# Performance work log

Measured on AMD Instinct MI355X. Metric: run time of the kernel, lower is better.

## Reference

```python
import jax, jax.numpy as jnp
import numpy as np

B, S, HID = 1, 2048, 4096
NH, NKV = 32, 8
HD = HID // NH          # 128
N_REP = NH // NKV       # 4
ROPE_THETA = 10000.0


def setup_inputs() -> dict:
    key = jax.random.key(0)
    ks = jax.random.split(key, 5)
    scale = 0.02
    x = jax.random.normal(ks[0], (B, S, HID), dtype=jnp.float32)
    Wq = jax.random.normal(ks[1], (HID, HID), dtype=jnp.float32) * scale
    Wk = jax.random.normal(ks[2], (NKV * HD, HID), dtype=jnp.float32) * scale
    Wv = jax.random.normal(ks[3], (NKV * HD, HID), dtype=jnp.float32) * scale
    Wo = jax.random.normal(ks[4], (HID, HID), dtype=jnp.float32) * scale
    position_ids = jnp.broadcast_to(jnp.arange(S, dtype=jnp.int32)[None, :], (B, S))
    return {"x": x, "Wq": Wq, "Wk": Wk, "Wv": Wv, "Wo": Wo, "position_ids": position_ids}


def _rope_cache(seq_len, dtype):
    inv_freq = 1.0 / (ROPE_THETA ** (jnp.arange(0, HD, 2, dtype=jnp.float32) / HD))
    t = jnp.arange(seq_len, dtype=jnp.float32)
    freqs = t[:, None] * inv_freq[None, :]            # [S, HD/2]
    emb = jnp.concatenate([freqs, freqs], axis=-1)    # [S, HD]
    return jnp.cos(emb).astype(dtype), jnp.sin(emb).astype(dtype)


def _rotate_half(x):
    x1, x2 = x[..., : HD // 2], x[..., HD // 2:]
    return jnp.concatenate([-x2, x1], axis=-1)


def reference(x, Wq, Wk, Wv, Wo, position_ids):
    b, s, _ = x.shape
    # projections (nn.Linear: x @ W.T)
    q = (x @ Wq.T).reshape(b, s, NH, HD).transpose(0, 2, 1, 3)    # [B,NH,S,HD]
    k = (x @ Wk.T).reshape(b, s, NKV, HD).transpose(0, 2, 1, 3)   # [B,NKV,S,HD]
    v = (x @ Wv.T).reshape(b, s, NKV, HD).transpose(0, 2, 1, 3)
    # RoPE
    cos_c, sin_c = _rope_cache(s, x.dtype)
    cos = cos_c[position_ids][:, None, :, :]   # [B,1,S,HD]
    sin = sin_c[position_ids][:, None, :, :]
    q = q * cos + _rotate_half(q) * sin
    k = k * cos + _rotate_half(k) * sin
    # GQA repeat_kv
    k = jnp.repeat(k, N_REP, axis=1)   # [B,NH,S,HD]
    v = jnp.repeat(v, N_REP, axis=1)
    # scaled dot-product attention with causal mask
    scores = jnp.einsum('bhqd,bhkd->bhqk', q, k) / jnp.sqrt(jnp.float32(HD))
    causal = jnp.tril(jnp.ones((s, s), dtype=bool))
    scores = jnp.where(causal[None, None, :, :], scores, jnp.finfo(scores.dtype).min)
    attn = jax.nn.softmax(scores.astype(jnp.float32), axis=-1).astype(q.dtype)
    out = jnp.einsum('bhqk,bhkd->bhqd', attn, v)                  # [B,NH,S,HD]
    out = out.transpose(0, 2, 1, 3).reshape(b, s, NH * HD)
    return out @ Wo.T
```

## Files before the change

kernel.cpp:

```cpp
#include <hip/hip_runtime.h>
#include <hip/hip_bf16.h>

#define DEVI __device__ __forceinline__

typedef __attribute__((ext_vector_type(8))) __bf16 bf16x8;
typedef __attribute__((ext_vector_type(4))) float f32x4;

DEVI f32x4 mfma_16x16x32(bf16x8 a, bf16x8 b, f32x4 c) {
  return __builtin_amdgcn_mfma_f32_16x16x32_bf16(a, b, c, 0, 0, 0);
}

DEVI void gld16(const void* g, void* l) {
  __builtin_amdgcn_global_load_lds(
      reinterpret_cast<const __attribute__((address_space(1))) unsigned int*>(
          reinterpret_cast<unsigned long long>(g)),
      reinterpret_cast<__attribute__((address_space(3))) unsigned int*>(
          reinterpret_cast<unsigned long long>(l)),
      16, 0, 0);
}

DEVI unsigned short f2bf(float f) {
  unsigned u = __builtin_bit_cast(unsigned, f);
  u += 0x7FFFu + ((u >> 16) & 1u);
  return (unsigned short)(u >> 16);
}
DEVI float bf2f(unsigned short b) {
  return __builtin_bit_cast(float, (unsigned)b << 16);
}

struct Conv5 {
  const float4 *x, *wq, *wk, *wv, *wo;
  ushort4 *xb, *wqkv, *wob;
};
__global__ void k_conv_all(Conv5 a) {
  constexpr int C0 = 2097152;
  constexpr int C1 = C0 + 4194304;
  constexpr int C2 = C1 + 1048576;
  constexpr int C3 = C2 + 1048576;
  constexpr int C4 = C3 + 4194304;
  int stride = gridDim.x * blockDim.x;
  for (int i = blockIdx.x * blockDim.x + threadIdx.x; i < C4; i += stride) {
    const float4* src; ushort4* dst; int j;
    if (i < C0)      { src = a.x;  dst = a.xb;             j = i; }
    else if (i < C1) { src = a.wq; dst = a.wqkv;           j = i - C0; }
    else if (i < C2) { src = a.wk; dst = a.wqkv + 4194304; j = i - C1; }
    else if (i < C3) { src = a.wv; dst = a.wqkv + 5242880; j = i - C2; }
    else             { src = a.wo; dst = a.wob;            j = i - C3; }
    float4 v = src[j];
    ushort4 o; o.x = f2bf(v.x); o.y = f2bf(v.y); o.z = f2bf(v.z); o.w = f2bf(v.w);
    dst[j] = o;
  }
}

__global__ void k_rope_table(float2* __restrict__ tab) {
  int idx = blockIdx.x * blockDim.x + threadIdx.x;
  int s = idx >> 6, d = idx & 63;
  float invf = powf(10000.0f, -(float)d * (1.0f / 64.0f));
  float f = (float)s * invf;
  tab[idx] = make_float2(cosf(f), sinf(f));
}

template <int NH_, int L2NH>
__global__ void k_rope_v(unsigned short* __restrict__ X, const float2* __restrict__ tab,
                         const int* __restrict__ pos, float scale) {
  int t = blockIdx.x * blockDim.x + threadIdx.x;
  int d0 = (t & 7) * 8;
  int sh = t >> 3;
  int s  = sh >> L2NH;
  int h  = sh & (NH_ - 1);
  size_t base = (size_t)s * (NH_ * 128) + h * 128 + d0;
  const float4* tf = (const float4*)(tab + (size_t)pos[s] * 64 + d0);
  unsigned short a[8], b[8], oa[8], ob[8];
  *(ushort4*)&a[0] = *(const ushort4*)(X + base);
  *(ushort4*)&a[4] = *(const ushort4*)(X + base + 4);
  *(ushort4*)&b[0] = *(const ushort4*)(X + base + 64);
  *(ushort4*)&b[4] = *(const ushort4*)(X + base + 68);
#pragma unroll
  for (int j = 0; j < 4; ++j) {
    float4 cs = tf[j];
    float x1 = bf2f(a[2*j]),   x2 = bf2f(b[2*j]);
    float y1 = bf2f(a[2*j+1]), y2 = bf2f(b[2*j+1]);
    oa[2*j]   = f2bf((x1 * cs.x - x2 * cs.y) * scale);
    ob[2*j]   = f2bf((x2 * cs.x + x1 * cs.y) * scale);
    oa[2*j+1] = f2bf((y1 * cs.z - y2 * cs.w) * scale);
    ob[2*j+1] = f2bf((y2 * cs.z + y1 * cs.w) * scale);
  }
  *(ushort4*)(X + base)      = *(ushort4*)&oa[0];
  *(ushort4*)(X + base + 4)  = *(ushort4*)&oa[4];
  *(ushort4*)(X + base + 64) = *(ushort4*)&ob[0];
  *(ushort4*)(X + base + 68) = *(ushort4*)&ob[4];
}

template <int EPI>
__global__ __launch_bounds__(256, 2)
void k_gemm64(const unsigned short* __restrict__ A,
              const unsigned short* __restrict__ B,
              void* __restrict__ Cp,
              unsigned short* __restrict__ Kp,
              unsigned short* __restrict__ Vtp,
              int K) {
  __shared__ __align__(16) unsigned short As[128][64];
  __shared__ __align__(16) unsigned short Bs[128][64];
  const int tid  = threadIdx.x;
  const int lane = tid & 63;
  const int wave = tid >> 6;
  const int bm = blockIdx.y * 128;
  const int bn = blockIdx.x * 128;
  const int wm = (wave >> 1) * 64;
  const int wn = (wave & 1) * 64;
  const int l15 = lane & 15;
  const int lg  = lane >> 4;

  f32x4 acc[4][4] = {};

  const int srow  = lane >> 3;
  const int scol  = ((lane & 7) ^ srow) * 8;
  const unsigned short* aS = A + (size_t)(bm + wave * 32 + srow) * K + scol;
  const unsigned short* bS = B + (size_t)(bn + wave * 32 + srow) * K + scol;

  for (int k0 = 0; k0 < K; k0 += 64) {
    __syncthreads();
#pragma unroll
    for (int c = 0; c < 4; ++c) {
      gld16(aS + (size_t)(c * 8) * K + k0, &As[wave * 32 + c * 8][0]);
      gld16(bS + (size_t)(c * 8) * K + k0, &Bs[wave * 32 + c * 8][0]);
    }
    __syncthreads();

#pragma unroll
    for (int ks = 0; ks < 2; ++ks) {
      bf16x8 a[4], b[4];
#pragma unroll
      for (int m = 0; m < 4; ++m)
        a[m] = *(const bf16x8*)&As[wm + m * 16 + l15][((ks * 4 + lg) ^ (l15 & 7)) * 8];
#pragma unroll
      for (int n = 0; n < 4; ++n)
        b[n] = *(const bf16x8*)&Bs[wn + n * 16 + l15][((ks * 4 + lg) ^ (l15 & 7)) * 8];
#pragma unroll
      for (int m = 0; m < 4; ++m)
#pragma unroll
        for (int n = 0; n < 4; ++n)
          acc[m][n] = mfma_16x16x32(a[m], b[n], acc[m][n]);
    }
  }

#pragma unroll
  for (int m = 0; m < 4; ++m)
#pragma unroll
    for (int n = 0; n < 4; ++n)
#pragma unroll
      for (int r = 0; r < 4; ++r) {
        int row = bm + wm + m * 16 + lg * 4 + r;
        int col = bn + wn + n * 16 + l15;
        float v = acc[m][n][r];
        if (EPI == 0) {
          if (col < 4096)      ((unsigned short*)Cp)[(size_t)row * 4096 + col] = f2bf(v);
          else if (col < 5120) Kp[(size_t)row * 1024 + (col - 4096)] = f2bf(v);
          else                 Vtp[(size_t)(col - 5120) * 2048 + row] = f2bf(v);
        } else {
          ((float*)Cp)[(size_t)row * 4096 + col] = v;
        }
      }
}

__global__ __launch_bounds__(256, 2)
void k_attn(const unsigned short* __restrict__ Q,
            const unsigned short* __restrict__ Kb,
            const unsigned short* __restrict__ Vt,
            unsigned short* __restrict__ AO) {
  __shared__ __align__(16) unsigned short Kl[2][64][128];
  __shared__ __align__(16) unsigned short Vl[2][128][64];
  __shared__ __align__(16) unsigned short Pl[4][16][72];
  const int tid = threadIdx.x, lane = tid & 63, w = tid >> 6;
  const int bid = blockIdx.x;
  const int qi = 31 - (bid >> 5);
  const int h  = bid & 31;
  const int q0 = qi * 64;
  const int kh = h >> 2;
  const int l15 = lane & 15, lg = lane >> 4;

  bf16x8 qf[4];
  {
    const unsigned short* qr = Q + (size_t)(q0 + w * 16 + l15) * 4096 + h * 128;
#pragma unroll
    for (int ks = 0; ks < 4; ++ks) qf[ks] = *(const bf16x8*)(qr + ks * 32 + lg * 8);
  }

  f32x4 o[8] = {};
  float m_run = -1e30f, l_run = 0.f;
  const int nkb = qi + 1;
  const int myq = q0 + w * 16 + l15;

  auto stageK = [&](int buf, int kv0) {
#pragma unroll
    for (int c = 0; c < 4; ++c) {
      int row = 16 * w + 4 * c + lg;
      gld16(Kb + (size_t)(kv0 + row) * 1024 + kh * 128 + ((l15 ^ (row & 7)) * 8),
            &Kl[buf][16 * w + 4 * c][0]);
    }
  };
  auto stageV = [&](int buf, int kv0) {
#pragma unroll
    for (int c = 0; c < 4; ++c) {
      int row = 32 * w + 8 * c + (lane >> 3);
      gld16(Vt + (size_t)(kh * 128 + row) * 2048 + kv0 + (((lane & 7) ^ (row & 7)) * 8),
            &Vl[buf][32 * w + 8 * c][0]);
    }
  };

  stageK(0, 0);
  stageV(0, 0);
  int cur = 0;

  for (int kb = 0; kb < nkb; ++kb) {
    const int kv0 = kb * 64;
    __syncthreads();
    if (kb + 1 < nkb) { stageK(cur ^ 1, kv0 + 64); stageV(cur ^ 1, kv0 + 64); }

    f32x4 s[4] = {};
    __builtin_amdgcn_s_setprio(1);
#pragma unroll
    for (int ks = 0; ks < 4; ++ks)
#pragma unroll
      for (int n = 0; n < 4; ++n) {
        bf16x8 bk = *(const bf16x8*)&Kl[cur][n * 16 + l15][((ks * 4 + lg) ^ (l15 & 7)) * 8];
        s[n] = mfma_16x16x32(bk, qf[ks], s[n]);
      }
    __builtin_amdgcn_s_setprio(0);

    if (kb == nkb - 1) {
#pragma unroll
      for (int n = 0; n < 4; ++n)
#pragma unroll
        for (int r = 0; r < 4; ++r)
          if (kv0 + n * 16 + lg * 4 + r > myq) s[n][r] = -1e30f;
    }

    float mx = -1e30f;
#pragma unroll
    for (int n = 0; n < 4; ++n)
      mx = fmaxf(mx, fmaxf(fmaxf(s[n][0], s[n][1]), fmaxf(s[n][2], s[n][3])));
    mx = fmaxf(mx, __shfl_xor(mx, 16));
    mx = fmaxf(mx, __shfl_xor(mx, 32));

    if (!__all(mx <= m_run + 8.0f)) {
      float mn = fmaxf(m_run, mx);
      float fac = __expf(m_run - mn);
      m_run = mn;
      l_run *= fac;
#pragma unroll
      for (int j = 0; j < 8; ++j) {
        o[j][0] *= fac; o[j][1] *= fac; o[j][2] *= fac; o[j][3] *= fac;
      }
    }
    float rs = 0.f;
#pragma unroll
    for (int n = 0; n < 4; ++n)
#pragma unroll
      for (int r = 0; r < 4; ++r) {
        float pv = __expf(s[n][r] - m_run);
        s[n][r] = pv;
        rs += pv;
      }
    rs += __shfl_xor(rs, 16);
    rs += __shfl_xor(rs, 32);
    l_run += rs;

#pragma unroll
    for (int n = 0; n < 4; ++n) {
      ushort4 pk;
      pk.x = f2bf(s[n][0]); pk.y = f2bf(s[n][1]); pk.z = f2bf(s[n][2]); pk.w = f2bf(s[n][3]);
      *(ushort4*)&Pl[w][l15][n * 16 + lg * 4] = pk;
    }
    asm volatile("s_waitcnt lgkmcnt(0)" ::: "memory");
    bf16x8 pa0 = *(const bf16x8*)&Pl[w][l15][lg * 8];
    bf16x8 pa1 = *(const bf16x8*)&Pl[w][l15][32 + lg * 8];

    __builtin_amdgcn_s_setprio(1);
#pragma unroll
    for (int j = 0; j < 8; ++j) {
      bf16x8 bv0 = *(const bf16x8*)&Vl[cur][j * 16 + l15][(lg ^ (l15 & 7)) * 8];
      bf16x8 bv1 = *(const bf16x8*)&Vl[cur][j * 16 + l15][((4 + lg) ^ (l15 & 7)) * 8];
      o[j] = mfma_16x16x32(bv0, pa0, o[j]);
      o[j] = mfma_16x16x32(bv1, pa1, o[j]);
    }
    __builtin_amdgcn_s_setprio(0);
    cur ^= 1;
  }

  float inv = 1.0f / l_run;
  __syncthreads();
  unsigned short* Ol = &Kl[0][0][0];
#pragma unroll
  for (int j = 0; j < 8; ++j)
#pragma unroll
    for (int r = 0; r < 4; ++r)
      Ol[w * 2176 + l15 * 136 + j * 16 + lg * 4 + r] = f2bf(o[j][r] * inv);
  asm volatile("s_waitcnt lgkmcnt(0)" ::: "memory");
#pragma unroll
  for (int p = 0; p < 4; ++p) {
    int row = p * 4 + lg;
    bf16x8 vv = *(const bf16x8*)&Ol[w * 2176 + row * 136 + l15 * 8];
    *(bf16x8*)(AO + (size_t)(q0 + w * 16 + row) * 4096 + h * 128 + l15 * 8) = vv;
  }
}

extern "C" void kernel_launch(void* const* d_in, const int* in_sizes, int n_in,
                              void* d_out, int out_size, void* d_ws, size_t ws_size,
                              hipStream_t stream) {
  const float* x  = (const float*)d_in[0];
  const float* Wq = (const float*)d_in[1];
  const float* Wk = (const float*)d_in[2];
  const float* Wv = (const float*)d_in[3];
  const float* Wo = (const float*)d_in[4];
  const int*   pos = (const int*)d_in[5];
  float* out = (float*)d_out;

  char* p = (char*)d_ws;
  unsigned short* xb   = (unsigned short*)p; p += (size_t)2048 * 4096 * 2;
  unsigned short* wqkv = (unsigned short*)p; p += (size_t)6144 * 4096 * 2;
  unsigned short* wob  = (unsigned short*)p; p += (size_t)4096 * 4096 * 2;
  unsigned short* qb   = (unsigned short*)p; p += (size_t)2048 * 4096 * 2;
  unsigned short* kb   = (unsigned short*)p; p += (size_t)2048 * 1024 * 2;
  unsigned short* vtb  = (unsigned short*)p; p += (size_t)1024 * 2048 * 2;
  unsigned short* aob  = (unsigned short*)p; p += (size_t)2048 * 4096 * 2;
  float2*         tab  = (float2*)p;         p += (size_t)2048 * 64 * 8;

  Conv5 ca;
  ca.x  = (const float4*)x;  ca.wq = (const float4*)Wq; ca.wk = (const float4*)Wk;
  ca.wv = (const float4*)Wv; ca.wo = (const float4*)Wo;
  ca.xb = (ushort4*)xb; ca.wqkv = (ushort4*)wqkv; ca.wob = (ushort4*)wob;
  k_conv_all<<<4096, 256, 0, stream>>>(ca);
  k_rope_table<<<512, 256, 0, stream>>>(tab);

  k_gemm64<0><<<dim3(48, 16), 256, 0, stream>>>(xb, wqkv, qb, kb, vtb, 4096);

  const float scale = 0.08838834764831845f;
  k_rope_v<32, 5><<<2048, 256, 0, stream>>>(qb, tab, pos, scale);
  k_rope_v<8, 3><<<512, 256, 0, stream>>>(kb, tab, pos, 1.0f);

  k_attn<<<1024, 256, 0, stream>>>(qb, kb, vtb, aob);

  k_gemm64<1><<<dim3(32, 16), 256, 0, stream>>>(aob, wob, out, nullptr, nullptr, 4096);
}
```

Before: 479.7 us.

## Process two 64-row query tiles per attention block to reuse staged K/V tiles

Each attention workgroup now handles 128 query rows as two 64-row halves that share every K/V tile staged in LDS. This halves the LDS staging and global K/V traffic per query row and halves the grid size. The first half skips its MFMAs on the final, fully masked key block. The P scratch buffer also gets an XOR swizzle in place of padding. The cost is doubled accumulator registers, which may hurt occupancy under launch_bounds(256,2), and fewer blocks (512) with more uneven causal work per block.

```diff
diff --git a/kernel.cpp b/kernel.cpp
--- a/kernel.cpp
+++ b/kernel.cpp
@@ -170,26 +170,32 @@
             unsigned short* __restrict__ AO) {
   __shared__ __align__(16) unsigned short Kl[2][64][128];
   __shared__ __align__(16) unsigned short Vl[2][128][64];
-  __shared__ __align__(16) unsigned short Pl[4][16][72];
+  __shared__ __align__(16) unsigned short Pl[4][2][16][64];
   const int tid = threadIdx.x, lane = tid & 63, w = tid >> 6;
   const int bid = blockIdx.x;
-  const int qi = 31 - (bid >> 5);
+  const int qi = 15 - (bid >> 5);
   const int h  = bid & 31;
-  const int q0 = qi * 64;
+  const int q0 = qi * 128;
   const int kh = h >> 2;
   const int l15 = lane & 15, lg = lane >> 4;
-
-  bf16x8 qf[4];
+  const int swz = (l15 & 7);
+
+  bf16x8 qf0[4], qf1[4];
   {
-    const unsigned short* qr = Q + (size_t)(q0 + w * 16 + l15) * 4096 + h * 128;
-#pragma unroll
-    for (int ks = 0; ks < 4; ++ks) qf[ks] = *(const bf16x8*)(qr + ks * 32 + lg * 8);
-  }
-
-  f32x4 o[8] = {};
-  float m_run = -1e30f, l_run = 0.f;
-  const int nkb = qi + 1;
-  const int myq = q0 + w * 16 + l15;
+    const unsigned short* qr0 = Q + (size_t)(q0 + w * 16 + l15) * 4096 + h * 128;
+    const unsigned short* qr1 = qr0 + (size_t)64 * 4096;
+#pragma unroll
+    for (int ks = 0; ks < 4; ++ks) {
+      qf0[ks] = *(const bf16x8*)(qr0 + ks * 32 + lg * 8);
+      qf1[ks] = *(const bf16x8*)(qr1 + ks * 32 + lg * 8);
+    }
+  }
+
+  f32x4 o0[8] = {}, o1[8] = {};
+  float m0 = -1e30f, l0 = 0.f, m1 = -1e30f, l1 = 0.f;
+  const int nkb  = 2 * qi + 2;
+  const int myq0 = q0 + w * 16 + l15;
+  const int myq1 = myq0 + 64;
 
   auto stageK = [&](int buf, int kv0) {
 #pragma unroll
@@ -217,91 +223,150 @@
     __syncthreads();
     if (kb + 1 < nkb) { stageK(cur ^ 1, kv0 + 64); stageV(cur ^ 1, kv0 + 64); }
 
-    f32x4 s[4] = {};
+    const bool skip0 = (kb == nkb - 1);
+    const bool maskt = (kb >= nkb - 2);
+
+    f32x4 s0[4] = {}, s1[4] = {};
     __builtin_amdgcn_s_setprio(1);
 #pragma unroll
     for (int ks = 0; ks < 4; ++ks)
 #pragma unroll
       for (int n = 0; n < 4; ++n) {
-        bf16x8 bk = *(const bf16x8*)&Kl[cur][n * 16 + l15][((ks * 4 + lg) ^ (l15 & 7)) * 8];
-        s[n] = mfma_16x16x32(bk, qf[ks], s[n]);
+        bf16x8 bk = *(const bf16x8*)&Kl[cur][n * 16 + l15][((ks * 4 + lg) ^ swz) * 8];
+        if (!skip0) s0[n] = mfma_16x16x32(bk, qf0[ks], s0[n]);
+        s1[n] = mfma_16x16x32(bk, qf1[ks], s1[n]);
       }
     __builtin_amdgcn_s_setprio(0);
 
-    if (kb == nkb - 1) {
-#pragma unroll
-      for (int n = 0; n < 4; ++n)
-#pragma unroll
-        for (int r = 0; r < 4; ++r)
-          if (kv0 + n * 16 + lg * 4 + r > myq) s[n][r] = -1e30f;
-    }
-
-    float mx = -1e30f;
-#pragma unroll
-    for (int n = 0; n < 4; ++n)
-      mx = fmaxf(mx, fmaxf(fmaxf(s[n][0], s[n][1]), fmaxf(s[n][2], s[n][3])));
-    mx = fmaxf(mx, __shfl_xor(mx, 16));
-    mx = fmaxf(mx, __shfl_xor(mx, 32));
-
-    if (!__all(mx <= m_run + 8.0f)) {
-      float mn = fmaxf(m_run, mx);
-      float fac = __expf(m_run - mn);
-      m_run = mn;
-      l_run *= fac;
-#pragma unroll
-      for (int j = 0; j < 8; ++j) {
-        o[j][0] *= fac; o[j][1] *= fac; o[j][2] *= fac; o[j][3] *= fac;
-      }
-    }
-    float rs = 0.f;
-#pragma unroll
-    for (int n = 0; n < 4; ++n)
-#pragma unroll
-      for (int r = 0; r < 4; ++r) {
-        float pv = __expf(s[n][r] - m_run);
-        s[n][r] = pv;
-        rs += pv;
-      }
-    rs += __shfl_xor(rs, 16);
-    rs += __shfl_xor(rs, 32);
-    l_run += rs;
-
-#pragma unroll
-    for (int n = 0; n < 4; ++n) {
-      ushort4 pk;
-      pk.x = f2bf(s[n][0]); pk.y = f2bf(s[n][1]); pk.z = f2bf(s[n][2]); pk.w = f2bf(s[n][3]);
-      *(ushort4*)&Pl[w][l15][n * 16 + lg * 4] = pk;
+    if (maskt) {
+#pragma unroll
+      for (int n = 0; n < 4; ++n)
+#pragma unroll
+        for (int r = 0; r < 4; ++r) {
+          int kv = kv0 + n * 16 + lg * 4 + r;
+          if (!skip0 && kv > myq0) s0[n][r] = -1e30f;
+          if (kv > myq1)           s1[n][r] = -1e30f;
+        }
+    }
+
+    if (!skip0) {
+      float mx = -1e30f;
+#pragma unroll
+      for (int n = 0; n < 4; ++n)
+        mx = fmaxf(mx, fmaxf(fmaxf(s0[n][0], s0[n][1]), fmaxf(s0[n][2], s0[n][3])));
+      mx = fmaxf(mx, __shfl_xor(mx, 16));
+      mx = fmaxf(mx, __shfl_xor(mx, 32));
+      if (!__all(mx <= m0 + 8.0f)) {
+        float mn = fmaxf(m0, mx);
+        float fac = __expf(m0 - mn);
+        m0 = mn; l0 *= fac;
+#pragma unroll
+        for (int j = 0; j < 8; ++j) {
+          o0[j][0] *= fac; o0[j][1] *= fac; o0[j][2] *= fac; o0[j][3] *= fac;
+        }
+      }
+      float rs = 0.f;
+#pragma unroll
+      for (int n = 0; n < 4; ++n)
+#pragma unroll
+        for (int r = 0; r < 4; ++r) {
+          float pv = __expf(s0[n][r] - m0);
+          s0[n][r] = pv; rs += pv;
+        }
+      rs += __shfl_xor(rs, 16);
+      rs += __shfl_xor(rs, 32);
+      l0 += rs;
+#pragma unroll
+      for (int n = 0; n < 4; ++n) {
+        ushort4 pk;
+        pk.x = f2bf(s0[n][0]); pk.y = f2bf(s0[n][1]);
+        pk.z = f2bf(s0[n][2]); pk.w = f2bf(s0[n][3]);
+        *(ushort4*)&Pl[w][0][l15][(((2 * n + (lg >> 1)) ^ swz) << 3) + ((lg & 1) << 2)] = pk;
+      }
+    }
+    {
+      float mx = -1e30f;
+#pragma unroll
+      for (int n = 0; n < 4; ++n)
+        mx = fmaxf(mx, fmaxf(fmaxf(s1[n][0], s1[n][1]), fmaxf(s1[n][2], s1[n][3])));
+      mx = fmaxf(mx, __shfl_xor(mx, 16));
+      mx = fmaxf(mx, __shfl_xor(mx, 32));
+      if (!__all(mx <= m1 + 8.0f)) {
+        float mn = fmaxf(m1, mx);
+        float fac = __expf(m1 - mn);
+        m1 = mn; l1 *= fac;
+#pragma unroll
+        for (int j = 0; j < 8; ++j) {
+          o1[j][0] *= fac; o1[j][1] *= fac; o1[j][2] *= fac; o1[j][3] *= fac;
+        }
+      }
+      float rs = 0.f;
+#pragma unroll
+      for (int n = 0; n < 4; ++n)
+#pragma unroll
+        for (int r = 0; r < 4; ++r) {
+          float pv = __expf(s1[n][r] - m1);
+          s1[n][r] = pv; rs += pv;
+        }
+      rs += __shfl_xor(rs, 16);
+      rs += __shfl_xor(rs, 32);
+      l1 += rs;
+#pragma unroll
+      for (int n = 0; n < 4; ++n) {
+        ushort4 pk;
+        pk.x = f2bf(s1[n][0]); pk.y = f2bf(s1[n][1]);
+        pk.z = f2bf(s1[n][2]); pk.w = f2bf(s1[n][3]);
+        *(ushort4*)&Pl[w][1][l15][(((2 * n + (lg >> 1)) ^ swz) << 3) + ((lg & 1) << 2)] = pk;
+      }
     }
     asm volatile("s_waitcnt lgkmcnt(0)" ::: "memory");
-    bf16x8 pa0 = *(const bf16x8*)&Pl[w][l15][lg * 8];
-    bf16x8 pa1 = *(const bf16x8*)&Pl[w][l15][32 + lg * 8];
+
+    bf16x8 pa00, pa01;
+    if (!skip0) {
+      pa00 = *(const bf16x8*)&Pl[w][0][l15][(lg ^ swz) << 3];
+      pa01 = *(const bf16x8*)&Pl[w][0][l15][((4 + lg) ^ swz) << 3];
+    }
+    bf16x8 pa10 = *(const bf16x8*)&Pl[w][1][l15][(lg ^ swz) << 3];
+    bf16x8 pa11 = *(const bf16x8*)&Pl[w][1][l15][((4 + lg) ^ swz) << 3];
 
     __builtin_amdgcn_s_setprio(1);
 #pragma unroll
     for (int j = 0; j < 8; ++j) {
-      bf16x8 bv0 = *(const bf16x8*)&Vl[cur][j * 16 + l15][(lg ^ (l15 & 7)) * 8];
-      bf16x8 bv1 = *(const bf16x8*)&Vl[cur][j * 16 + l15][((4 + lg) ^ (l15 & 7)) * 8];
-      o[j] = mfma_16x16x32(bv0, pa0, o[j]);
-      o[j] = mfma_16x16x32(bv1, pa1, o[j]);
+      bf16x8 bv0 = *(const bf16x8*)&Vl[cur][j * 16 + l15][(lg ^ swz) * 8];
+      bf16x8 bv1 = *(const bf16x8*)&Vl[cur][j * 16 + l15][((4 + lg) ^ swz) * 8];
+      if (!skip0) {
+        o0[j] = mfma_16x16x32(bv0, pa00, o0[j]);
+        o0[j] = mfma_16x16x32(bv1, pa01, o0[j]);
+      }
+      o1[j] = mfma_16x16x32(bv0, pa10, o1[j]);
+      o1[j] = mfma_16x16x32(bv1, pa11, o1[j]);
     }
     __builtin_amdgcn_s_setprio(0);
     cur ^= 1;
   }
 
-  float inv = 1.0f / l_run;
+  float inv0 = 1.0f / l0, inv1 = 1.0f / l1;
   __syncthreads();
-  unsigned short* Ol = &Kl[0][0][0];
-#pragma unroll
-  for (int j = 0; j < 8; ++j)
-#pragma unroll
-    for (int r = 0; r < 4; ++r)
-      Ol[w * 2176 + l15 * 136 + j * 16 + lg * 4 + r] = f2bf(o[j][r] * inv);
+  unsigned short* O0 = &Kl[0][0][0];
+  unsigned short* O1 = &Vl[0][0][0];
+#pragma unroll
+  for (int j = 0; j < 8; ++j) {
+    ushort4 t0, t1;
+    t0.x = f2bf(o0[j][0] * inv0); t0.y = f2bf(o0[j][1] * inv0);
+    t0.z = f2bf(o0[j][2] * inv0); t0.w = f2bf(o0[j][3] * inv0);
+    t1.x = f2bf(o1[j][0] * inv1); t1.y = f2bf(o1[j][1] * inv1);
+    t1.z = f2bf(o1[j][2] * inv1); t1.w = f2bf(o1[j][3] * inv1);
+    *(ushort4*)&O0[w * 2176 + l15 * 136 + j * 16 + lg * 4] = t0;
+    *(ushort4*)&O1[w * 2176 + l15 * 136 + j * 16 + lg * 4] = t1;
+  }
   asm volatile("s_waitcnt lgkmcnt(0)" ::: "memory");
 #pragma unroll
   for (int p = 0; p < 4; ++p) {
     int row = p * 4 + lg;
-    bf16x8 vv = *(const bf16x8*)&Ol[w * 2176 + row * 136 + l15 * 8];
-    *(bf16x8*)(AO + (size_t)(q0 + w * 16 + row) * 4096 + h * 128 + l15 * 8) = vv;
+    bf16x8 v0 = *(const bf16x8*)&O0[w * 2176 + row * 136 + l15 * 8];
+    bf16x8 v1 = *(const bf16x8*)&O1[w * 2176 + row * 136 + l15 * 8];
+    *(bf16x8*)(AO + (size_t)(q0 + w * 16 + row) * 4096 + h * 128 + l15 * 8) = v0;
+    *(bf16x8*)(AO + (size_t)(q0 + 64 + w * 16 + row) * 4096 + h * 128 + l15 * 8) = v1;
   }
 }
 
@@ -339,7 +404,7 @@
   k_rope_v<32, 5><<<2048, 256, 0, stream>>>(qb, tab, pos, scale);
   k_rope_v<8, 3><<<512, 256, 0, stream>>>(kb, tab, pos, 1.0f);
 
-  k_attn<<<1024, 256, 0, stream>>>(qb, kb, vtb, aob);
+  k_attn<<<512, 256, 0, stream>>>(qb, kb, vtb, aob);
 
   k_gemm64<1><<<dim3(32, 16), 256, 0, stream>>>(aob, wob, out, nullptr, nullptr, 4096);
 }
```

New measurement: 522.3 us. +8.9%, slower.
